# Optimization experiments

Measured on AMD Instinct MI355X. Metric: run time of the kernel, lower is better.

The kernel has to match this reference:

```python
import jax, jax.numpy as jnp
import numpy as np


def setup_inputs() -> dict:
    key = jax.random.key(0)
    k1, k2 = jax.random.split(key)
    x = jax.random.normal(k1, (8, 8192, 512), dtype=jnp.float32)
    W_proj = jax.random.normal(k2, (512, 128), dtype=jnp.float32) * (1.0 / np.sqrt(512.0))
    perm_weights = jnp.ones((128,), dtype=jnp.float32)
    return {"x": x, "W_proj": W_proj, "perm_weights": perm_weights}


def reference(x, W_proj, perm_weights):
    # x: (b, n, d_in) -> project to (b, n, d_red)
    x_proj = jnp.einsum('bnd,dr->bnr', x, W_proj)
    # mean over all n cyclic shifts == global mean along seq axis, broadcast
    # back to every position (exact identity of the original roll/stack loop)
    seq_mean = jnp.mean(x_proj, axis=1, keepdims=True)          # (b, 1, d_red)
    x_reynolds = jnp.broadcast_to(seq_mean, x_proj.shape)       # (b, n, d_red)
    return x_reynolds * perm_weights
```

## Files before the change

kernel.cpp:

```cpp
#include <hip/hip_runtime.h>

#define B_ 8
#define N_ 8192
#define D_ 512
#define R_ 128

__global__ __launch_bounds__(512) void k_reduce_proj(const float* __restrict__ x,
                                                     const float* __restrict__ W,
                                                     float* __restrict__ partial_y,
                                                     int chunks) {
    const int rows  = N_ / chunks;
    const int b     = blockIdx.x / chunks;
    const int chunk = blockIdx.x % chunks;
    const int t  = threadIdx.x;
    const int dq = t & 127;
    const int rp = t >> 7;

    const float4* x4 = reinterpret_cast<const float4*>(x)
                       + ((size_t)b * N_ + (size_t)chunk * rows) * (D_ / 4);

    float4 acc = make_float4(0.f, 0.f, 0.f, 0.f);
    for (int n = rp; n < rows; n += 4) {
        float4 v = x4[(size_t)n * (D_ / 4) + dq];
        acc.x += v.x; acc.y += v.y; acc.z += v.z; acc.w += v.w;
    }

    __shared__ float4 s[512];
    __shared__ float  xs[D_];
    __shared__ float  red[512];

    s[t] = acc;
    __syncthreads();
    if (rp == 0) {
        float4 a1 = s[dq + 128], a2 = s[dq + 256], a3 = s[dq + 384];
        float4 r;
        r.x = (acc.x + a1.x) + (a2.x + a3.x);
        r.y = (acc.y + a1.y) + (a2.y + a3.y);
        r.z = (acc.z + a1.z) + (a2.z + a3.z);
        r.w = (acc.w + a1.w) + (a2.w + a3.w);
        reinterpret_cast<float4*>(xs)[dq] = r;
    }
    __syncthreads();

    const int r128 = t & 127;
    const int g    = t >> 7;
    float accd = 0.f;
    #pragma unroll 8
    for (int d0 = 0; d0 < 128; ++d0) {
        const int d = g * 128 + d0;
        accd = fmaf(xs[d], W[(size_t)d * R_ + r128], accd);
    }
    red[t] = accd;
    __syncthreads();
    if (g == 0) {
        float v = (red[r128] + red[r128 + 128]) + (red[r128 + 256] + red[r128 + 384]);
        partial_y[((size_t)(b * chunks + chunk)) * R_ + r128] = v;
    }
}

__global__ __launch_bounds__(256) void k_sumbcast(const float* __restrict__ partial_y,
                                                  const float* __restrict__ perm,
                                                  float* __restrict__ out,
                                                  int chunks) {
    const int b  = blockIdx.x >> 7;
    const int rb = blockIdx.x & 127;
    const int t  = threadIdx.x;
    const int r    = t & 127;
    const int half = t >> 7;

    __shared__ float red[256];
    __shared__ float yv[R_];

    const int ch = chunks >> 1;
    const float* p = partial_y + ((size_t)b * chunks + (size_t)half * ch) * R_ + r;
    float s = 0.f;
    #pragma unroll 8
    for (int c = 0; c < ch; ++c)
        s += p[(size_t)c * R_];
    red[t] = s;
    __syncthreads();
    if (half == 0)
        yv[r] = (red[r] + red[r + 128]) * perm[r] * (1.0f / (float)N_);
    __syncthreads();

    const int q  = t & 31;
    const int rp = t >> 5;
    const float4 val = reinterpret_cast<const float4*>(yv)[q];
    float4* out4 = reinterpret_cast<float4*>(out)
                   + ((size_t)b * N_ + (size_t)rb * 64) * (R_ / 4);
    #pragma unroll
    for (int n = rp; n < 64; n += 8)
        out4[(size_t)n * (R_ / 4) + q] = val;
}

extern "C" void kernel_launch(void* const* d_in, const int* in_sizes, int n_in,
                              void* d_out, int out_size, void* d_ws, size_t ws_size,
                              hipStream_t stream) {
    const float* x    = (const float*)d_in[0];
    const float* W    = (const float*)d_in[1];
    const float* perm = (const float*)d_in[2];
    float* out = (float*)d_out;

    int chunks = 64;
    while (chunks > 2 &&
           (size_t)(B_ * chunks * R_) * sizeof(float) > ws_size)
        chunks >>= 1;

    float* partial_y = (float*)d_ws;

    k_reduce_proj<<<dim3(B_ * chunks), dim3(512), 0, stream>>>(x, W, partial_y, chunks);
    k_sumbcast  <<<dim3(B_ * (N_ / 64)), dim3(256), 0, stream>>>(partial_y, perm, out, chunks);
}
```

Measured before the change: 37.38 us.

## Fuse reduce-project and broadcast kernels with a grid-wide atomic barrier

```diff
diff --git a/kernel.cpp b/kernel.cpp
--- a/kernel.cpp
+++ b/kernel.cpp
@@ -4,35 +4,40 @@
 #define N_ 8192
 #define D_ 512
 #define R_ 128
+#define CHUNKS_ 64
+#define ROWS_ 128
+#define GRID_ (B_ * CHUNKS_)
 
-__global__ __launch_bounds__(512) void k_reduce_proj(const float* __restrict__ x,
-                                                     const float* __restrict__ W,
-                                                     float* __restrict__ partial_y,
-                                                     int chunks) {
-    const int rows  = N_ / chunks;
-    const int b     = blockIdx.x / chunks;
-    const int chunk = blockIdx.x % chunks;
+__global__ __launch_bounds__(512) void k_fused(const float* __restrict__ x,
+                                               const float* __restrict__ W,
+                                               const float* __restrict__ perm,
+                                               float* __restrict__ partial_y,
+                                               unsigned int* __restrict__ counter,
+                                               float* __restrict__ out) {
+    const int b  = blockIdx.x >> 6;
+    const int ck = blockIdx.x & (CHUNKS_ - 1);
     const int t  = threadIdx.x;
+
+    __shared__ float4 s4[512];
+    __shared__ float  xs[D_];
+    __shared__ float  red[512];
+    __shared__ float  yv[R_];
+
     const int dq = t & 127;
     const int rp = t >> 7;
-
     const float4* x4 = reinterpret_cast<const float4*>(x)
-                       + ((size_t)b * N_ + (size_t)chunk * rows) * (D_ / 4);
+                       + ((size_t)b * N_ + (size_t)ck * ROWS_) * (D_ / 4);
 
     float4 acc = make_float4(0.f, 0.f, 0.f, 0.f);
-    for (int n = rp; n < rows; n += 4) {
+    #pragma unroll 8
+    for (int n = rp; n < ROWS_; n += 4) {
         float4 v = x4[(size_t)n * (D_ / 4) + dq];
         acc.x += v.x; acc.y += v.y; acc.z += v.z; acc.w += v.w;
     }
-
-    __shared__ float4 s[512];
-    __shared__ float  xs[D_];
-    __shared__ float  red[512];
-
-    s[t] = acc;
+    s4[t] = acc;
     __syncthreads();
     if (rp == 0) {
-        float4 a1 = s[dq + 128], a2 = s[dq + 256], a3 = s[dq + 384];
+        float4 a1 = s4[dq + 128], a2 = s4[dq + 256], a3 = s4[dq + 384];
         float4 r;
         r.x = (acc.x + a1.x) + (a2.x + a3.x);
         r.y = (acc.y + a1.y) + (a2.y + a3.y);
@@ -42,54 +47,54 @@
     }
     __syncthreads();
 
-    const int r128 = t & 127;
-    const int g    = t >> 7;
-    float accd = 0.f;
+    const int r = t & 127;
+    const int g = t >> 7;
+    float a = 0.f;
     #pragma unroll 8
     for (int d0 = 0; d0 < 128; ++d0) {
         const int d = g * 128 + d0;
-        accd = fmaf(xs[d], W[(size_t)d * R_ + r128], accd);
+        a = fmaf(xs[d], W[(size_t)d * R_ + r], a);
     }
-    red[t] = accd;
+    red[t] = a;
     __syncthreads();
     if (g == 0) {
-        float v = (red[r128] + red[r128 + 128]) + (red[r128 + 256] + red[r128 + 384]);
-        partial_y[((size_t)(b * chunks + chunk)) * R_ + r128] = v;
+        float v = (red[r] + red[r + 128]) + (red[r + 256] + red[r + 384]);
+        partial_y[(size_t)blockIdx.x * R_ + r] = v;
     }
-}
+    __syncthreads();
 
-__global__ __launch_bounds__(256) void k_sumbcast(const float* __restrict__ partial_y,
-                                                  const float* __restrict__ perm,
-                                                  float* __restrict__ out,
-                                                  int chunks) {
-    const int b  = blockIdx.x >> 7;
-    const int rb = blockIdx.x & 127;
-    const int t  = threadIdx.x;
-    const int r    = t & 127;
-    const int half = t >> 7;
+    if (t == 0) {
+        __threadfence();
+        atomicAdd(counter, 1u);
+        while (__hip_atomic_load(counter, __ATOMIC_ACQUIRE,
+                                 __HIP_MEMORY_SCOPE_AGENT) < (unsigned)GRID_) {
+            __builtin_amdgcn_s_sleep(8);
+        }
+        __threadfence();
+    }
+    __syncthreads();
 
-    __shared__ float red[256];
-    __shared__ float yv[R_];
-
-    const int ch = chunks >> 1;
-    const float* p = partial_y + ((size_t)b * chunks + (size_t)half * ch) * R_ + r;
+    const int q4 = t >> 7;
+    const float* p = partial_y
+                     + ((size_t)b * CHUNKS_ + (size_t)q4 * (CHUNKS_ / 4)) * R_ + r;
     float s = 0.f;
     #pragma unroll 8
-    for (int c = 0; c < ch; ++c)
+    for (int c = 0; c < CHUNKS_ / 4; ++c)
         s += p[(size_t)c * R_];
     red[t] = s;
     __syncthreads();
-    if (half == 0)
-        yv[r] = (red[r] + red[r + 128]) * perm[r] * (1.0f / (float)N_);
+    if (q4 == 0)
+        yv[r] = ((red[r] + red[r + 128]) + (red[r + 256] + red[r + 384]))
+                * perm[r] * (1.0f / (float)N_);
     __syncthreads();
 
-    const int q  = t & 31;
-    const int rp = t >> 5;
+    const int q   = t & 31;
+    const int rp2 = t >> 5;
     const float4 val = reinterpret_cast<const float4*>(yv)[q];
     float4* out4 = reinterpret_cast<float4*>(out)
-                   + ((size_t)b * N_ + (size_t)rb * 64) * (R_ / 4);
+                   + ((size_t)b * N_ + (size_t)ck * ROWS_) * (R_ / 4);
     #pragma unroll
-    for (int n = rp; n < 64; n += 8)
+    for (int n = rp2; n < ROWS_; n += 16)
         out4[(size_t)n * (R_ / 4) + q] = val;
 }
 
@@ -101,13 +106,9 @@
     const float* perm = (const float*)d_in[2];
     float* out = (float*)d_out;
 
-    int chunks = 64;
-    while (chunks > 2 &&
-           (size_t)(B_ * chunks * R_) * sizeof(float) > ws_size)
-        chunks >>= 1;
+    unsigned int* counter = (unsigned int*)d_ws;
+    float* partial_y = (float*)((char*)d_ws + 256);
 
-    float* partial_y = (float*)d_ws;
-
-    k_reduce_proj<<<dim3(B_ * chunks), dim3(512), 0, stream>>>(x, W, partial_y, chunks);
-    k_sumbcast  <<<dim3(B_ * (N_ / 64)), dim3(256), 0, stream>>>(partial_y, perm, out, chunks);
+    hipMemsetAsync(counter, 0, sizeof(unsigned int), stream);
+    k_fused<<<dim3(GRID_), dim3(512), 0, stream>>>(x, W, perm, partial_y, counter, out);
 }
```

After: 112.6 us. +201.3%, slower.
